# Optimization experiments

Measured on AMD Instinct MI355X. Metric: run time of the kernel, lower is better.

Reference implementation:

```python
import jax, jax.numpy as jnp
import numpy as np

B, C, H, W = 64, 3, 224, 224
DEPTH = 2
NUM_OPS = 14

def _lin(m, lo, hi):
    return lo + m * (hi - lo)

def _clip255(x):
    return jnp.clip(x, 0.0, 255.0)

def _affine_sample(img, a, b, c, d, e, f):
    # img: [C,H,W]; inverse map (x_out,y_out)->(a*x+b*y+c, d*x+e*y+f); bilinear, zero fill.
    ch, h, w = img.shape
    ys, xs = jnp.meshgrid(jnp.arange(h, dtype=img.dtype), jnp.arange(w, dtype=img.dtype), indexing='ij')
    sx = a * xs + b * ys + c
    sy = d * xs + e * ys + f
    x0 = jnp.floor(sx); y0 = jnp.floor(sy)
    wx = sx - x0; wy = sy - y0
    def gather(yi, xi):
        valid = (xi >= 0) & (xi <= w - 1) & (yi >= 0) & (yi <= h - 1)
        v = img[:, jnp.clip(yi, 0, h - 1).astype(jnp.int32), jnp.clip(xi, 0, w - 1).astype(jnp.int32)]
        return jnp.where(valid[None], v, 0.0)
    v00 = gather(y0, x0); v01 = gather(y0, x0 + 1)
    v10 = gather(y0 + 1, x0); v11 = gather(y0 + 1, x0 + 1)
    top = v00 * (1 - wx) + v01 * wx
    bot = v10 * (1 - wx) + v11 * wx
    return top * (1 - wy) + bot * wy

def _gray(img):
    lum = jnp.array([0.299, 0.587, 0.114], img.dtype)
    return jnp.einsum('chw,c->hw', img, lum)

def shear_x(img, m):
    v = _lin(m, -0.3, 0.3)
    return _affine_sample(img, 1.0, v, 0.0, 0.0, 1.0, 0.0)

def shear_y(img, m):
    v = _lin(m, -0.3, 0.3)
    return _affine_sample(img, 1.0, 0.0, 0.0, v, 1.0, 0.0)

def translate_x(img, m):
    v = _lin(m, -0.45, 0.45) * img.shape[2]
    return _affine_sample(img, 1.0, 0.0, v, 0.0, 1.0, 0.0)

def translate_y(img, m):
    v = _lin(m, -0.45, 0.45) * img.shape[1]
    return _affine_sample(img, 1.0, 0.0, 0.0, 0.0, 1.0, v)

def rotate(img, m):
    rad = _lin(m, -30.0, 30.0) * np.pi / 180.0
    cx = (img.shape[2] - 1) * 0.5
    cy = (img.shape[1] - 1) * 0.5
    cs, sn = jnp.cos(rad), jnp.sin(rad)
    c = cx - cs * cx - sn * cy
    f = cy + sn * cx - cs * cy
    return _affine_sample(img, cs, sn, c, -sn, cs, f)

def brightness(img, m):
    return _clip255(img * _lin(m, 0.1, 1.9))

def color(img, m):
    g = _gray(img)[None]
    return _clip255(g + _lin(m, 0.1, 1.9) * (img - g))

def sharpness(img, m):
    k = jnp.array([[1., 1., 1.], [1., 5., 1.], [1., 1., 1.]], img.dtype) / 13.0
    ch = img.shape[0]
    kern = jnp.tile(k[None, None], (ch, 1, 1, 1))  # [C,1,3,3] depthwise
    blur = jax.lax.conv_general_dilated(img[None], kern, (1, 1), 'SAME', feature_group_count=ch)[0]
    out = _clip255(blur + _lin(m, 0.1, 1.9) * (img - blur))
    # PIL keeps the 1-px border unchanged
    out = out.at[:, 0, :].set(img[:, 0, :]).at[:, -1, :].set(img[:, -1, :])
    out = out.at[:, :, 0].set(img[:, :, 0]).at[:, :, -1].set(img[:, :, -1])
    return out

def contrast(img, m):
    mu = jnp.mean(_gray(img))
    return _clip255(mu + _lin(m, 0.1, 1.9) * (img - mu))

def solarize(img, m):
    thr = _lin(m, 0.0, 256.0)
    return jnp.where(img < thr, img, 255.0 - img)

def posterize(img, m):
    nbits = jnp.round(_lin(m, 0.0, 4.0))  # bits removed -> keep 8-nbits
    q = 2.0 ** nbits
    return jnp.floor(img / q) * q

def equalize(img, m):
    def eq_ch(chan):
        v = jnp.clip(jnp.round(chan), 0, 255).astype(jnp.int32)
        hist = jnp.zeros(256, jnp.int32).at[v.ravel()].add(1)
        step = (jnp.sum(hist) - hist[255]) // 255
        cum = jnp.concatenate([jnp.zeros(1, jnp.int32), jnp.cumsum(hist)[:-1]])
        lut = jnp.where(step > 0,
                        jnp.clip((cum + step // 2) // jnp.maximum(step, 1), 0, 255),
                        jnp.arange(256))
        return lut[v].astype(chan.dtype)
    return jax.vmap(eq_ch)(img)

def autocontrast(img, m):
    lo = jnp.min(img, axis=(1, 2), keepdims=True)
    hi = jnp.max(img, axis=(1, 2), keepdims=True)
    scale = 255.0 / jnp.maximum(hi - lo, 1e-6)
    return jnp.where(hi > lo, _clip255((img - lo) * scale), img)

def identity(img, m):
    return img

BRANCHES = [shear_x, shear_y, translate_x, translate_y, rotate, brightness, color,
            sharpness, contrast, solarize, posterize, equalize, autocontrast, identity]

def setup_inputs() -> dict:
    key = jax.random.key(0)
    k1, k2, k3, k4, k5 = jax.random.split(key, 5)
    x = jax.random.uniform(k1, (B, C, H, W), jnp.float32)          # [0,1]; module scales by 255
    ra_deform = jax.random.uniform(k2, (DEPTH, B), jnp.float32)    # magnitudes in [0,1]
    op_idx = jax.random.randint(k3, (DEPTH, B), 0, NUM_OPS, jnp.int32)
    p = jax.random.uniform(k4, (DEPTH, B), jnp.float32, 0.2, 0.8)  # p_min_t..p_max_t
    apply_mask = jax.random.uniform(k5, (DEPTH, B), jnp.float32) < p
    return {"x": x, "ra_deform": ra_deform, "op_idx": op_idx, "apply_mask": apply_mask}

def reference(x, ra_deform, op_idx, apply_mask):
    x = x * jnp.where(jnp.max(x) <= 1.0, 255.0, 1.0)
    x = x.astype(jnp.float32)
    def apply_one(img, j, m, ap):
        out = jax.lax.switch(j, BRANCHES, img, m)
        return jnp.where(ap, out, img)
    for i in range(DEPTH):  # small fixed depth
        x = jax.vmap(apply_one)(x, op_idx[i], ra_deform[i], apply_mask[i])
    return jnp.clip(x / 255.0, 0.0, 1.0)
```

## Files before the change

### kernel.cpp

```cpp
#include <hip/hip_runtime.h>

#define WID 224
#define HGT 224
#define HWp 50176
#define CHW 150528
#define NB  64
#define NSL 2048
#define SCH 1568
#define NT  9408
#define TPI 147
#define TPC 49

#define OFF_MAXB   0
#define OFF_HIST1  256
#define OFF_PSUM0  49408
#define OFF_PMIN0  51456
#define OFF_PMAX0  57600
#define OFF_PHIST0 63744
#define OFF_PSUM1  3209472
#define OFF_PMIN1  3247104
#define OFF_PMAX1  3284736
#define OFF_INTER  3322368

__device__ __forceinline__ float clip255(float v){ return fminf(fmaxf(v, 0.f), 255.f); }

__device__ __forceinline__ float wred(float v, int op){
    #pragma unroll
    for (int o = 32; o > 0; o >>= 1){
        float u = __shfl_down(v, o);
        v = (op==0) ? v+u : (op==1 ? fminf(v,u) : fmaxf(v,u));
    }
    return v;
}

__device__ __forceinline__ float blk_reduce(float v, float* red, int tid, int op){
    float w = wred(v, op);
    if ((tid & 63) == 0) red[tid >> 6] = w;
    __syncthreads();
    float a = red[0], b = red[1], c = red[2], d = red[3];
    float r = (op==0) ? (a+b)+(c+d) : (op==1 ? fminf(fminf(a,b),fminf(c,d)) : fmaxf(fmaxf(a,b),fmaxf(c,d)));
    __syncthreads();
    return r;
}

__device__ __forceinline__ const float* lut_scan(int hv, int* shh, float* slut, int tid, int* h255){
    if (tid == 255) *h255 = hv;
    shh[tid] = hv;
    __syncthreads();
    #pragma unroll
    for (int off = 1; off < 256; off <<= 1){
        int v = (tid >= off) ? shh[tid-off] : 0;
        __syncthreads();
        shh[tid] += v;
        __syncthreads();
    }
    int cum = shh[tid] - hv;
    int step = (HWp - *h255) / 255;
    int l = (step > 0) ? min(max((cum + (step >> 1)) / step, 0), 255) : tid;
    slut[tid] = (float)l;
    __syncthreads();
    return slut;
}

__device__ __forceinline__ float samp(const float* __restrict__ pl, float yi, float xi, float scl){
    if (xi < 0.f || xi > (float)(WID-1) || yi < 0.f || yi > (float)(HGT-1)) return 0.f;
    return pl[(int)yi * WID + (int)xi] * scl;
}

__device__ __forceinline__ void apply_body(const float* __restrict__ img,
                                           int c, int p,
                                           int j, int ap, float m, float scl,
                                           float mu, float lo, float hi,
                                           const float* lut,
                                           float o[4])
{
    int y = p / WID;
    int x = p - y*WID;
    const float* pl = img + c*HWp;
    float4 v4 = *(const float4*)(pl + p);
    float iv[4] = {v4.x*scl, v4.y*scl, v4.z*scl, v4.w*scl};

    if (!ap) {
        #pragma unroll
        for (int k = 0; k < 4; k++) o[k] = iv[k];
        return;
    }
    switch (j){
    case 0: case 1: case 2: case 3: case 4: {
        float a = 1.f, bb = 0.f, cc = 0.f, dd = 0.f, ee = 1.f, ff = 0.f;
        if (j == 0)      bb = -0.3f + 0.6f*m;
        else if (j == 1) dd = -0.3f + 0.6f*m;
        else if (j == 2) cc = (-0.45f + 0.9f*m) * (float)WID;
        else if (j == 3) ff = (-0.45f + 0.9f*m) * (float)HGT;
        else {
            float deg = -30.f + 60.f*m;
            float rad = deg * (float)(3.14159265358979323846/180.0);
            float cs = cosf(rad), sn = sinf(rad);
            float cx = (WID-1)*0.5f, cy = (HGT-1)*0.5f;
            a = cs; bb = sn; dd = -sn; ee = cs;
            cc = cx - cs*cx - sn*cy;
            ff = cy + sn*cx - cs*cy;
        }
        float yf = (float)y;
        #pragma unroll
        for (int k = 0; k < 4; k++){
            float xf = (float)(x + k);
            float sx = a*xf + bb*yf + cc;
            float sy = dd*xf + ee*yf + ff;
            float x0f = floorf(sx), y0f = floorf(sy);
            float wx = sx - x0f, wy = sy - y0f;
            float v00 = samp(pl, y0f,     x0f,     scl);
            float v01 = samp(pl, y0f,     x0f+1.f, scl);
            float v10 = samp(pl, y0f+1.f, x0f,     scl);
            float v11 = samp(pl, y0f+1.f, x0f+1.f, scl);
            float top = v00*(1.f-wx) + v01*wx;
            float bot = v10*(1.f-wx) + v11*wx;
            o[k] = top*(1.f-wy) + bot*wy;
        }
        break; }
    case 5: {
        float f = 0.1f + 1.8f*m;
        #pragma unroll
        for (int k = 0; k < 4; k++) o[k] = clip255(iv[k]*f);
        break; }
    case 6: {
        float4 r4 = *(const float4*)(img + p);
        float4 g4 = *(const float4*)(img + HWp + p);
        float4 b4 = *(const float4*)(img + 2*HWp + p);
        float rr[4] = {r4.x*scl, r4.y*scl, r4.z*scl, r4.w*scl};
        float gg[4] = {g4.x*scl, g4.y*scl, g4.z*scl, g4.w*scl};
        float bl[4] = {b4.x*scl, b4.y*scl, b4.z*scl, b4.w*scl};
        float f = 0.1f + 1.8f*m;
        #pragma unroll
        for (int k = 0; k < 4; k++){
            float g = 0.299f*rr[k] + 0.587f*gg[k] + 0.114f*bl[k];
            o[k] = clip255(g + f*(iv[k] - g));
        }
        break; }
    case 7: {
        float f = 0.1f + 1.8f*m;
        #pragma unroll
        for (int k = 0; k < 4; k++){
            int xx = x + k;
            if (y == 0 || y == HGT-1 || xx == 0 || xx == WID-1) o[k] = iv[k];
            else {
                int q = p + k;
                float s8 = pl[q-WID-1] + pl[q-WID] + pl[q-WID+1]
                         + pl[q-1]     + pl[q+1]
                         + pl[q+WID-1] + pl[q+WID] + pl[q+WID+1];
                float blur = (s8*scl + 5.f*iv[k]) * (1.f/13.f);
                o[k] = clip255(blur + f*(iv[k] - blur));
            }
        }
        break; }
    case 8: {
        float f = 0.1f + 1.8f*m;
        #pragma unroll
        for (int k = 0; k < 4; k++) o[k] = clip255(mu + f*(iv[k] - mu));
        break; }
    case 9: {
        float thr = 256.f*m;
        #pragma unroll
        for (int k = 0; k < 4; k++) o[k] = (iv[k] < thr) ? iv[k] : 255.f - iv[k];
        break; }
    case 10: {
        float q = exp2f(rintf(4.f*m));
        #pragma unroll
        for (int k = 0; k < 4; k++) o[k] = floorf(iv[k]/q)*q;
        break; }
    case 11: {
        #pragma unroll
        for (int k = 0; k < 4; k++){
            int ivi = min(max((int)rintf(iv[k]), 0), 255);
            o[k] = lut[ivi];
        }
        break; }
    case 12: {
        float sc = 255.f / fmaxf(hi - lo, 1e-6f);
        #pragma unroll
        for (int k = 0; k < 4; k++)
            o[k] = (hi > lo) ? clip255((iv[k] - lo) * sc) : iv[k];
        break; }
    default:
        #pragma unroll
        for (int k = 0; k < 4; k++) o[k] = iv[k];
        break;
    }
}

__global__ void k1_stats(const float* __restrict__ x, const int* __restrict__ op,
                         const int* __restrict__ mask, float* __restrict__ wsf)
{
    __shared__ float red[4];
    __shared__ int sh[1536];
    int* ints = (int*)wsf;
    float* psum0 = wsf + OFF_PSUM0;
    float* pmin0 = wsf + OFF_PMIN0;
    float* pmax0 = wsf + OFF_PMAX0;
    int* phist0 = (int*)wsf + OFF_PHIST0;
    int* hist1  = (int*)wsf + OFF_HIST1;

    int bid = blockIdx.x, tid = threadIdx.x;
    int blk = ((bid & 7) << 8) + (bid >> 3);
    if (tid < 24) hist1[blk*24 + tid] = 0;

    int b = blk >> 5, s = blk & 31;
    int j = op[b], ap = mask[b];
    bool needSum  = ap && (j == 8);
    bool needMM   = ap && (j == 12);
    bool needHist = ap && (j == 11);
    const float* img = x + (size_t)b * CHW;
    int p0 = s * SCH;
    const float GW[3] = {0.299f, 0.587f, 0.114f};

    float mx = 0.f, gs = 0.f;
    for (int c = 0; c < 3; c++){
        const float* pl = img + c*HWp + p0;
        float lo = 3.4e38f, hi = 0.f, cs = 0.f;
        for (int p = tid*4; p < SCH; p += 1024){
            float4 v = *(const float4*)(pl + p);
            float m4 = fmaxf(fmaxf(v.x, v.y), fmaxf(v.z, v.w));
            mx = fmaxf(mx, m4);
            if (needMM){ hi = fmaxf(hi, m4); lo = fminf(lo, fminf(fminf(v.x,v.y), fminf(v.z,v.w))); }
            if (needSum) cs += (v.x + v.y) + (v.z + v.w);
        }
        if (needSum) gs += GW[c] * cs;
        if (needMM){
            float l = blk_reduce(lo, red, tid, 1);
            if (!tid) pmin0[blk*3 + c] = l;
            float h = blk_reduce(hi, red, tid, 2);
            if (!tid) pmax0[blk*3 + c] = h;
        }
    }
    float bm = blk_reduce(mx, red, tid, 2);
    if (!tid) atomicMax(&ints[OFF_MAXB], __float_as_int(bm));
    if (needSum){
        float t = blk_reduce(gs, red, tid, 0);
        if (!tid) psum0[blk] = t;
    }
    if (needHist){
        for (int i = tid; i < 1536; i += 256) sh[i] = 0;
        __syncthreads();
        for (int c = 0; c < 3; c++){
            const float* pl = img + c*HWp + p0;
            for (int p = tid; p < SCH; p += 256){
                float v = pl[p];
                atomicAdd(&sh[c*256 + min(max((int)rintf(v), 0), 255)], 1);
                atomicAdd(&sh[768 + c*256 + min(max((int)rintf(v*255.f), 0), 255)], 1);
            }
        }
        __syncthreads();
        for (int i = tid; i < 1536; i += 256) phist0[blk*1536 + i] = sh[i];
    }
}

__global__ void k2_apply0(const float* __restrict__ x, const float* __restrict__ ra,
                          const int* __restrict__ op, const int* __restrict__ mask,
                          float* __restrict__ wsf)
{
    __shared__ float red[4];
    __shared__ int   shh[256];
    __shared__ float slut[256];
    __shared__ int   h255;
    const int* ints = (const int*)wsf;
    const float* psum0 = wsf + OFF_PSUM0;
    const float* pmin0 = wsf + OFF_PMIN0;
    const float* pmax0 = wsf + OFF_PMAX0;
    const int* phist0 = (const int*)wsf + OFF_PHIST0;
    int* hist1 = (int*)wsf + OFF_HIST1;
    float* psum1 = wsf + OFF_PSUM1;
    float* pmin1 = wsf + OFF_PMIN1;
    float* pmax1 = wsf + OFF_PMAX1;
    float* inter = wsf + OFF_INTER;

    int bid = blockIdx.x, tid = threadIdx.x;
    int t = ((bid & 7) * 1176) + (bid >> 3);
    int b = t / TPI;
    int r = t - b*TPI;
    int c = r / TPC;
    int p = (r - c*TPC)*1024 + tid*4;

    float scl = (__int_as_float(ints[OFF_MAXB]) <= 1.0f) ? 255.f : 1.f;
    int j = op[b], ap = mask[b];
    float m = ra[b];

    float mu = 0.f, lo = 0.f, hi = 0.f;
    const float* lut = nullptr;
    if (ap){
        if (j == 8){
            float v = (tid < 32) ? psum0[b*32 + tid] : 0.f;
            mu = blk_reduce(v, red, tid, 0) * scl * (1.f/(float)HWp);
        } else if (j == 12){
            float v  = (tid < 32) ? pmin0[(b*32 + tid)*3 + c] : 3.4e38f;
            lo = blk_reduce(v, red, tid, 1) * scl;
            float v2 = (tid < 32) ? pmax0[(b*32 + tid)*3 + c] : 0.f;
            hi = blk_reduce(v2, red, tid, 2) * scl;
        } else if (j == 11){
            int d = (scl == 255.f) ? 1 : 0;
            const int* ph = phist0 + d*768 + c*256 + tid;
            int sum = 0;
            #pragma unroll 8
            for (int s = 0; s < 32; s++) sum += ph[(b*32 + s)*1536];
            lut = lut_scan(sum, shh, slut, tid, &h255);
        }
    }

    float o[4];
    apply_body(x + (size_t)b*CHW, c, p, j, ap, m, scl, mu, lo, hi, lut, o);
    float4 w = {o[0], o[1], o[2], o[3]};
    *(float4*)(inter + (size_t)b*CHW + c*HWp + p) = w;

    int j1 = op[NB + b], ap1 = mask[NB + b];
    if (ap1 && (j1 == 8 || j1 == 11 || j1 == 12)){
        const float GW[3] = {0.299f, 0.587f, 0.114f};
        int wv = tid >> 6;
        if (j1 == 8){
            float s4 = (o[0] + o[1]) + (o[2] + o[3]);
            float ws = wred(s4, 0);
            if ((tid & 63) == 0) psum1[t*4 + wv] = ws * GW[c];
        } else if (j1 == 12){
            float l4 = fminf(fminf(o[0],o[1]), fminf(o[2],o[3]));
            float h4 = fmaxf(fmaxf(o[0],o[1]), fmaxf(o[2],o[3]));
            float wl = wred(l4, 1);
            float wh = wred(h4, 2);
            if ((tid & 63) == 0){ pmin1[t*4 + wv] = wl; pmax1[t*4 + wv] = wh; }
        } else {
            __syncthreads();
            shh[tid] = 0;
            __syncthreads();
            #pragma unroll
            for (int k = 0; k < 4; k++)
                atomicAdd(&shh[min(max((int)rintf(o[k]), 0), 255)], 1);
            __syncthreads();
            int v = shh[tid];
            if (v) atomicAdd(&hist1[b*768 + c*256 + tid], v);
        }
    }
}

__global__ void k3_apply1(const float* __restrict__ ra, const int* __restrict__ op,
                          const int* __restrict__ mask, float* __restrict__ out,
                          float* __restrict__ wsf)
{
    __shared__ float red[4];
    __shared__ int   shh[256];
    __shared__ float slut[256];
    __shared__ int   h255;
    const int* hist1 = (const int*)wsf + OFF_HIST1;
    const float* psum1 = wsf + OFF_PSUM1;
    const float* pmin1 = wsf + OFF_PMIN1;
    const float* pmax1 = wsf + OFF_PMAX1;
    const float* inter = wsf + OFF_INTER;

    int bid = blockIdx.x, tid = threadIdx.x;
    int t = ((bid & 7) * 1176) + (bid >> 3);
    int b = t / TPI;
    int r = t - b*TPI;
    int c = r / TPC;
    int p = (r - c*TPC)*1024 + tid*4;

    int j = op[NB + b], ap = mask[NB + b];
    float m = ra[NB + b];

    float mu = 0.f, lo = 0.f, hi = 0.f;
    const float* lut = nullptr;
    if (ap){
        if (j == 8){
            float v = 0.f;
            for (int i = tid; i < TPI*4; i += 256) v += psum1[b*TPI*4 + i];
            mu = blk_reduce(v, red, tid, 0) * (1.f/(float)HWp);
        } else if (j == 12){
            float v  = (tid < TPC*4) ? pmin1[(b*TPI + c*TPC)*4 + tid] : 3.4e38f;
            lo = blk_reduce(v, red, tid, 1);
            float v2 = (tid < TPC*4) ? pmax1[(b*TPI + c*TPC)*4 + tid] : 0.f;
            hi = blk_reduce(v2, red, tid, 2);
        } else if (j == 11){
            lut = lut_scan(hist1[b*768 + c*256 + tid], shh, slut, tid, &h255);
        }
    }

    float o[4];
    apply_body(inter + (size_t)b*CHW, c, p, j, ap, m, 1.f, mu, lo, hi, lut, o);
    float4 w;
    w.x = fminf(fmaxf(o[0]*(1.f/255.f), 0.f), 1.f);
    w.y = fminf(fmaxf(o[1]*(1.f/255.f), 0.f), 1.f);
    w.z = fminf(fmaxf(o[2]*(1.f/255.f), 0.f), 1.f);
    w.w = fminf(fmaxf(o[3]*(1.f/255.f), 0.f), 1.f);
    *(float4*)(out + (size_t)b*CHW + c*HWp + p) = w;
}

extern "C" void kernel_launch(void* const* d_in, const int* in_sizes, int n_in,
                              void* d_out, int out_size, void* d_ws, size_t ws_size,
                              hipStream_t stream) {
    const float* x    = (const float*)d_in[0];
    const float* ra   = (const float*)d_in[1];
    const int*   op   = (const int*)d_in[2];
    const int*   mask = (const int*)d_in[3];
    float* out = (float*)d_out;
    float* wsf = (float*)d_ws;

    k1_stats <<<NSL, 256, 0, stream>>>(x, op, mask, wsf);
    k2_apply0<<<NT,  256, 0, stream>>>(x, ra, op, mask, wsf);
    k3_apply1<<<NT,  256, 0, stream>>>(ra, op, mask, out, wsf);
}
```

Baseline: 154.8 us.

## Specialize geometric ops, vectorize sharpness stencil, hoist pixel load, drop XCD block swizzle

Shear-x and translate-x now fetch five contiguous row values and do 1D lerp, translate-y loads two float4 rows, and shear-y does a vertical-only lerp. This replaces the generic four-tap bilinear gather, cutting redundant loads and bounds checks. The sharpness stencil now reads neighbour rows as float4 and reuses values across the four outputs instead of issuing eight scalar loads per pixel. The centre pixel load is hoisted ahead of the stats reduction so its latency overlaps. Block-index swizzling for XCD locality is removed, which may change cache locality on the multi-die GPU.

```diff
diff --git a/kernel.cpp b/kernel.cpp
--- a/kernel.cpp
+++ b/kernel.cpp
@@ -68,7 +68,7 @@
 }
 
 __device__ __forceinline__ void apply_body(const float* __restrict__ img,
-                                           int c, int p,
+                                           int c, int p, float4 v4,
                                            int j, int ap, float m, float scl,
                                            float mu, float lo, float hi,
                                            const float* lut,
@@ -77,7 +77,7 @@
     int y = p / WID;
     int x = p - y*WID;
     const float* pl = img + c*HWp;
-    float4 v4 = *(const float4*)(pl + p);
+    float vr[4] = {v4.x, v4.y, v4.z, v4.w};
     float iv[4] = {v4.x*scl, v4.y*scl, v4.z*scl, v4.w*scl};
 
     if (!ap) {
@@ -86,21 +86,58 @@
         return;
     }
     switch (j){
-    case 0: case 1: case 2: case 3: case 4: {
-        float a = 1.f, bb = 0.f, cc = 0.f, dd = 0.f, ee = 1.f, ff = 0.f;
-        if (j == 0)      bb = -0.3f + 0.6f*m;
-        else if (j == 1) dd = -0.3f + 0.6f*m;
-        else if (j == 2) cc = (-0.45f + 0.9f*m) * (float)WID;
-        else if (j == 3) ff = (-0.45f + 0.9f*m) * (float)HGT;
-        else {
-            float deg = -30.f + 60.f*m;
-            float rad = deg * (float)(3.14159265358979323846/180.0);
-            float cs = cosf(rad), sn = sinf(rad);
-            float cx = (WID-1)*0.5f, cy = (HGT-1)*0.5f;
-            a = cs; bb = sn; dd = -sn; ee = cs;
-            cc = cx - cs*cx - sn*cy;
-            ff = cy + sn*cx - cs*cy;
-        }
+    case 0: case 2: {
+        float off = (j==0) ? (-0.3f + 0.6f*m)*(float)y
+                           : (-0.45f + 0.9f*m)*(float)WID;
+        float sx0 = (float)x + off;
+        float x0f = floorf(sx0);
+        float wx  = sx0 - x0f;
+        int   x0  = (int)x0f;
+        const float* row = pl + y*WID;
+        float v[5];
+        #pragma unroll
+        for (int k = 0; k < 5; k++){
+            int col = x0 + k;
+            v[k] = (col >= 0 && col < WID) ? row[col]*scl : 0.f;
+        }
+        #pragma unroll
+        for (int k = 0; k < 4; k++) o[k] = v[k]*(1.f-wx) + v[k+1]*wx;
+        break; }
+    case 3: {
+        float ff  = (-0.45f + 0.9f*m)*(float)HGT;
+        float sy0 = (float)y + ff;
+        float y0f = floorf(sy0);
+        float wy  = sy0 - y0f;
+        int   y0  = (int)y0f;
+        float4 t4 = {0.f,0.f,0.f,0.f}, b4 = {0.f,0.f,0.f,0.f};
+        if (y0   >= 0 && y0   < HGT) t4 = *(const float4*)(pl + y0*WID + x);
+        if (y0+1 >= 0 && y0+1 < HGT) b4 = *(const float4*)(pl + (y0+1)*WID + x);
+        float tt[4] = {t4.x,t4.y,t4.z,t4.w}, bb[4] = {b4.x,b4.y,b4.z,b4.w};
+        #pragma unroll
+        for (int k = 0; k < 4; k++) o[k] = (tt[k]*scl)*(1.f-wy) + (bb[k]*scl)*wy;
+        break; }
+    case 1: {
+        float dd = -0.3f + 0.6f*m;
+        #pragma unroll
+        for (int k = 0; k < 4; k++){
+            float sy = dd*(float)(x+k) + (float)y;
+            float y0f = floorf(sy);
+            float wy  = sy - y0f;
+            int   y0  = (int)y0f;
+            int col = x + k;
+            float tv = (y0   >= 0 && y0   < HGT) ? pl[y0*WID + col]*scl : 0.f;
+            float bv = (y0+1 >= 0 && y0+1 < HGT) ? pl[(y0+1)*WID + col]*scl : 0.f;
+            o[k] = tv*(1.f-wy) + bv*wy;
+        }
+        break; }
+    case 4: {
+        float deg = -30.f + 60.f*m;
+        float rad = deg * (float)(3.14159265358979323846/180.0);
+        float cs = cosf(rad), sn = sinf(rad);
+        float cx = (WID-1)*0.5f, cy = (HGT-1)*0.5f;
+        float a = cs, bb = sn, dd = -sn, ee = cs;
+        float cc = cx - cs*cx - sn*cy;
+        float ff = cy + sn*cx - cs*cy;
         float yf = (float)y;
         #pragma unroll
         for (int k = 0; k < 4; k++){
@@ -139,17 +176,28 @@
         break; }
     case 7: {
         float f = 0.1f + 1.8f*m;
-        #pragma unroll
-        for (int k = 0; k < 4; k++){
-            int xx = x + k;
-            if (y == 0 || y == HGT-1 || xx == 0 || xx == WID-1) o[k] = iv[k];
-            else {
-                int q = p + k;
-                float s8 = pl[q-WID-1] + pl[q-WID] + pl[q-WID+1]
-                         + pl[q-1]     + pl[q+1]
-                         + pl[q+WID-1] + pl[q+WID] + pl[q+WID+1];
-                float blur = (s8*scl + 5.f*iv[k]) * (1.f/13.f);
-                o[k] = clip255(blur + f*(iv[k] - blur));
+        if (y == 0 || y == HGT-1){
+            #pragma unroll
+            for (int k = 0; k < 4; k++) o[k] = iv[k];
+        } else {
+            float4 up4 = *(const float4*)(pl + p - WID);
+            float4 dn4 = *(const float4*)(pl + p + WID);
+            bool hasL = (x > 0), hasR = (x < WID-4);
+            float u0 = hasL ? pl[p-WID-1] : 0.f, u5 = hasR ? pl[p-WID+4] : 0.f;
+            float c0 = hasL ? pl[p-1]     : 0.f, c5 = hasR ? pl[p+4]     : 0.f;
+            float d0 = hasL ? pl[p+WID-1] : 0.f, d5 = hasR ? pl[p+WID+4] : 0.f;
+            float uu[6] = {u0, up4.x, up4.y, up4.z, up4.w, u5};
+            float cc[6] = {c0, vr[0], vr[1], vr[2], vr[3], c5};
+            float dd[6] = {d0, dn4.x, dn4.y, dn4.z, dn4.w, d5};
+            #pragma unroll
+            for (int k = 0; k < 4; k++){
+                int xx = x + k;
+                if (xx == 0 || xx == WID-1) o[k] = iv[k];
+                else {
+                    float s8 = uu[k]+uu[k+1]+uu[k+2] + cc[k]+cc[k+2] + dd[k]+dd[k+1]+dd[k+2];
+                    float blur = (s8*scl + 5.f*iv[k]) * (1.f/13.f);
+                    o[k] = clip255(blur + f*(iv[k] - blur));
+                }
             }
         }
         break; }
@@ -200,8 +248,7 @@
     int* phist0 = (int*)wsf + OFF_PHIST0;
     int* hist1  = (int*)wsf + OFF_HIST1;
 
-    int bid = blockIdx.x, tid = threadIdx.x;
-    int blk = ((bid & 7) << 8) + (bid >> 3);
+    int blk = blockIdx.x, tid = threadIdx.x;
     if (tid < 24) hist1[blk*24 + tid] = 0;
 
     int b = blk >> 5, s = blk & 31;
@@ -273,12 +320,14 @@
     float* pmax1 = wsf + OFF_PMAX1;
     float* inter = wsf + OFF_INTER;
 
-    int bid = blockIdx.x, tid = threadIdx.x;
-    int t = ((bid & 7) * 1176) + (bid >> 3);
+    int t = blockIdx.x, tid = threadIdx.x;
     int b = t / TPI;
     int r = t - b*TPI;
     int c = r / TPC;
     int p = (r - c*TPC)*1024 + tid*4;
+
+    const float* img = x + (size_t)b*CHW;
+    float4 v4 = *(const float4*)(img + c*HWp + p);
 
     float scl = (__int_as_float(ints[OFF_MAXB]) <= 1.0f) ? 255.f : 1.f;
     int j = op[b], ap = mask[b];
@@ -306,7 +355,7 @@
     }
 
     float o[4];
-    apply_body(x + (size_t)b*CHW, c, p, j, ap, m, scl, mu, lo, hi, lut, o);
+    apply_body(img, c, p, v4, j, ap, m, scl, mu, lo, hi, lut, o);
     float4 w = {o[0], o[1], o[2], o[3]};
     *(float4*)(inter + (size_t)b*CHW + c*HWp + p) = w;
 
@@ -352,12 +401,14 @@
     const float* pmax1 = wsf + OFF_PMAX1;
     const float* inter = wsf + OFF_INTER;
 
-    int bid = blockIdx.x, tid = threadIdx.x;
-    int t = ((bid & 7) * 1176) + (bid >> 3);
+    int t = blockIdx.x, tid = threadIdx.x;
     int b = t / TPI;
     int r = t - b*TPI;
     int c = r / TPC;
     int p = (r - c*TPC)*1024 + tid*4;
+
+    const float* img = inter + (size_t)b*CHW;
+    float4 v4 = *(const float4*)(img + c*HWp + p);
 
     int j = op[NB + b], ap = mask[NB + b];
     float m = ra[NB + b];
@@ -380,7 +431,7 @@
     }
 
     float o[4];
-    apply_body(inter + (size_t)b*CHW, c, p, j, ap, m, 1.f, mu, lo, hi, lut, o);
+    apply_body(img, c, p, v4, j, ap, m, 1.f, mu, lo, hi, lut, o);
     float4 w;
     w.x = fminf(fmaxf(o[0]*(1.f/255.f), 0.f), 1.f);
     w.y = fminf(fmaxf(o[1]*(1.f/255.f), 0.f), 1.f);
```

After: 145.1 us. 6.3% less time.
